# Performance work log

Hardware: AMD Instinct MI355X
Metric: run time of the kernel (lower is better)

Reference implementation:

```python
import jax, jax.numpy as jnp
import numpy as np

N = 50000        # num nodes
E = 1_600_000    # num edges
NNZ = 16         # sparse features per node
V = 100000       # feature vocabulary (num_total_features)
D = 128          # embedding_dim
H = 128          # hidden_dim
O = 64           # out_embedding_dim


def setup_inputs() -> dict:
    key = jax.random.key(0)
    ks = jax.random.split(key, 12)
    s = 0.05
    return {
        "feature_indices": jax.random.randint(ks[0], (N * NNZ,), 0, V, dtype=jnp.int32),
        "feature_offsets": jnp.arange(N, dtype=jnp.int32) * NNZ,
        "feature_weights": jax.random.uniform(ks[1], (N * NNZ,), dtype=jnp.float32),
        "edge_index": jax.random.randint(ks[2], (2, E), 0, N, dtype=jnp.int32),
        "noise": jax.random.normal(ks[3], (N, O), dtype=jnp.float32),
        "emb_table": jax.random.normal(ks[4], (V, D), dtype=jnp.float32) * s,
        "W1": jax.random.normal(ks[5], (D, H), dtype=jnp.float32) * s,
        "b1": jnp.zeros((H,), dtype=jnp.float32),
        "Wmu": jax.random.normal(ks[6], (H, O), dtype=jnp.float32) * s,
        "bmu": jnp.zeros((O,), dtype=jnp.float32),
        "Wls": jax.random.normal(ks[7], (H, O), dtype=jnp.float32) * s,
        "bls": jnp.zeros((O,), dtype=jnp.float32),
    }


def _gcn(x, W, b, src, dst, norm_e, deg_inv):
    # GCNConv with self-loops and symmetric normalization:
    # out_i = sum_{j->i} norm_ji * (W x_j) + deg_i^{-1} * (W x_i) + b
    xw = x @ W
    agg = jax.ops.segment_sum(norm_e[:, None] * xw[src], dst, num_segments=N)
    return agg + xw * deg_inv[:, None] + b


def reference(feature_indices, feature_offsets, feature_weights, edge_index, noise,
              emb_table, W1, b1, Wmu, bmu, Wls, bls):
    # --- EmbeddingBag(mode='sum') with per_sample_weights ---
    total = feature_indices.shape[0]
    bag_ids = jnp.searchsorted(feature_offsets, jnp.arange(total), side="right") - 1
    x = jax.ops.segment_sum(feature_weights[:, None] * emb_table[feature_indices],
                            bag_ids, num_segments=N)  # [N, D]
    # --- F.normalize(p=2, dim=-1) ---
    x = x / jnp.maximum(jnp.linalg.norm(x, axis=-1, keepdims=True), 1e-12)

    # --- shared GCN normalization (self-loops added) ---
    src, dst = edge_index[0], edge_index[1]
    deg = 1.0 + jax.ops.segment_sum(jnp.ones((E,), x.dtype), dst, num_segments=N)
    deg_isqrt = deg ** -0.5
    norm_e = deg_isqrt[src] * deg_isqrt[dst]  # per-edge norm
    deg_inv = 1.0 / deg                        # self-loop norm

    # --- encoder ---
    h = jax.nn.relu(_gcn(x, W1, b1, src, dst, norm_e, deg_inv))
    mu = _gcn(h, Wmu, bmu, src, dst, norm_e, deg_inv)
    logstd = _gcn(h, Wls, bls, src, dst, norm_e, deg_inv)
    z = mu + noise * jnp.exp(logstd)

    # --- dot-product decoder over edge_index ---
    logits = jnp.sum(z[src] * z[dst], axis=-1)  # [E]
    return logits
```

## Files before the change

### kernel.cpp

```cpp
#include <hip/hip_runtime.h>
#include <hip/hip_bf16.h>

constexpr int N_ = 50000;
constexpr int E_ = 1600000;
constexpr int D_ = 128;
constexpr int O_ = 64;
constexpr int NNZ_ = 16;
constexpr int V_ = 100000;
constexpr int NBIN_ = (N_ + 255) / 256;

static __device__ __forceinline__ unsigned short f2bf(float f) {
    __hip_bfloat16 h = __float2bfloat16(f);
    return __builtin_bit_cast(unsigned short, h);
}
static __device__ __forceinline__ unsigned int pack2(float a, float b) {
    return (unsigned int)f2bf(a) | ((unsigned int)f2bf(b) << 16);
}
static __device__ __forceinline__ float blo(unsigned int u) { return __uint_as_float(u << 16); }
static __device__ __forceinline__ float bhi(unsigned int u) { return __uint_as_float(u & 0xffff0000u); }
static __device__ __forceinline__ float4 fma4(float s, float4 a, float4 b) {
    return make_float4(fmaf(s, a.x, b.x), fmaf(s, a.y, b.y),
                       fmaf(s, a.z, b.z), fmaf(s, a.w, b.w));
}

__global__ __launch_bounds__(256) void k_cvt(const float* __restrict__ emb,
                                             unsigned int* __restrict__ emb_bf) {
    int t = blockIdx.x * blockDim.x + threadIdx.x;
    if (t >= V_ * D_ / 8) return;
    float4 a = ((const float4*)emb)[t * 2];
    float4 b = ((const float4*)emb)[t * 2 + 1];
    uint4 o;
    o.x = pack2(a.x, a.y);
    o.y = pack2(a.z, a.w);
    o.z = pack2(b.x, b.y);
    o.w = pack2(b.z, b.w);
    ((uint4*)emb_bf)[t] = o;
}

__global__ __launch_bounds__(256) void k_embed(const int* __restrict__ fi,
                                               const float* __restrict__ fw,
                                               const unsigned int* __restrict__ emb_bf,
                                               unsigned int* __restrict__ x) {
    int lane = threadIdx.x & 63;
    int h = lane >> 5, c = lane & 31;
    int n = blockIdx.x * 8 + ((threadIdx.x >> 6) << 1) + h;
    if (n >= N_) return;
    float a0 = 0.f, a1 = 0.f, a2 = 0.f, a3 = 0.f;
    int base = n * NNZ_;
#pragma unroll
    for (int j = 0; j < NNZ_; ++j) {
        int idx  = fi[base + j];
        float w  = fw[base + j];
        uint2 r = ((const uint2*)emb_bf)[(size_t)idx * 32 + c];
        a0 = fmaf(w, blo(r.x), a0);
        a1 = fmaf(w, bhi(r.x), a1);
        a2 = fmaf(w, blo(r.y), a2);
        a3 = fmaf(w, bhi(r.y), a3);
    }
    float ss = a0 * a0 + a1 * a1 + a2 * a2 + a3 * a3;
#pragma unroll
    for (int o = 16; o; o >>= 1) ss += __shfl_xor(ss, o);
    float sc = 1.0f / fmaxf(sqrtf(ss), 1e-12f);
    ((uint2*)x)[(size_t)n * 32 + c] =
        make_uint2(pack2(a0 * sc, a1 * sc), pack2(a2 * sc, a3 * sc));
}

constexpr int EPB_ = 8192;
__global__ __launch_bounds__(256) void k_bhist(const int* __restrict__ dst,
                                               int* __restrict__ bin_total) {
    __shared__ int hist[256];
    int t = threadIdx.x;
    hist[t] = 0;
    __syncthreads();
    int e0 = blockIdx.x * EPB_;
#pragma unroll
    for (int i = 0; i < EPB_ / 256; ++i) {
        int e = e0 + i * 256 + t;
        if (e < E_) atomicAdd(&hist[dst[e] >> 8], 1);
    }
    __syncthreads();
    if (t < NBIN_ && hist[t]) atomicAdd(&bin_total[t], hist[t]);
}

__global__ __launch_bounds__(256) void k_scan196(const int* __restrict__ bin_total,
                                                 int* __restrict__ coarse_start,
                                                 int* __restrict__ coarse_cursor,
                                                 int* __restrict__ row_start) {
    __shared__ int s[256];
    int t = threadIdx.x;
    int v = (t < NBIN_) ? bin_total[t] : 0;
    s[t] = v;
    __syncthreads();
    for (int o = 1; o < 256; o <<= 1) {
        int u = (t >= o) ? s[t - o] : 0;
        __syncthreads();
        s[t] += u;
        __syncthreads();
    }
    int excl = s[t] - v;
    if (t <= NBIN_) { coarse_start[t] = excl; coarse_cursor[t] = excl; }
    if (t == 0) row_start[N_] = E_;
}

__global__ __launch_bounds__(256) void k_bin(const int* __restrict__ src,
                                             const int* __restrict__ dst,
                                             int* __restrict__ coarse_cursor,
                                             unsigned int* __restrict__ binned) {
    __shared__ int hist[256], base[256];
    int t = threadIdx.x;
    int e0 = blockIdx.x * EPB_;
    hist[t] = 0;
    __syncthreads();
#pragma unroll
    for (int i = 0; i < EPB_ / 256; ++i) {
        int e = e0 + i * 256 + t;
        if (e < E_) atomicAdd(&hist[dst[e] >> 8], 1);
    }
    __syncthreads();
    if (t < NBIN_ && hist[t]) base[t] = atomicAdd(&coarse_cursor[t], hist[t]);
    __syncthreads();
#pragma unroll
    for (int i = 0; i < EPB_ / 256; ++i) {
        int e = e0 + i * 256 + t;
        if (e < E_) {
            int d = dst[e];
            int pos = atomicAdd(&base[d >> 8], 1);
            binned[pos] = (unsigned int)src[e] | ((unsigned int)(d & 255) << 16);
        }
    }
}

__global__ __launch_bounds__(256) void k_node(const unsigned int* __restrict__ binned,
                                              const int* __restrict__ coarse_start,
                                              float* __restrict__ disq,
                                              float* __restrict__ dinv,
                                              int* __restrict__ row_start) {
    __shared__ int hist[256], s[256];
    int t = threadIdx.x;
    hist[t] = 0;
    __syncthreads();
    int beg = coarse_start[blockIdx.x], end = coarse_start[blockIdx.x + 1];
    for (int j = beg + t; j < end; j += 256)
        atomicAdd(&hist[(binned[j] >> 16) & 255], 1);
    __syncthreads();
    int v = hist[t];
    int n = (blockIdx.x << 8) + t;
    if (n < N_) {
        float deg = 1.0f + (float)v;
        disq[n] = rsqrtf(deg);
        dinv[n] = 1.0f / deg;
    }
    s[t] = v;
    __syncthreads();
    for (int o = 1; o < 256; o <<= 1) {
        int u = (t >= o) ? s[t - o] : 0;
        __syncthreads();
        s[t] += u;
        __syncthreads();
    }
    if (n < N_) row_start[n] = beg + (s[t] - v);
}

__global__ __launch_bounds__(256) void k_fill2(const unsigned int* __restrict__ binned,
                                               const int* __restrict__ coarse_start,
                                               const int* __restrict__ row_start,
                                               int* __restrict__ sorted_src) {
    __shared__ int cur[256];
    int t = threadIdx.x;
    int n0 = blockIdx.x << 8;
    if (n0 + t < N_) cur[t] = row_start[n0 + t];
    __syncthreads();
    int beg = coarse_start[blockIdx.x], end = coarse_start[blockIdx.x + 1];
    for (int j = beg + t; j < end; j += 256) {
        unsigned int b = binned[j];
        int pos = atomicAdd(&cur[(b >> 16) & 255], 1);
        sorted_src[pos] = (int)(b & 0xFFFFu);
    }
}

__global__ __launch_bounds__(256) void k_gather(const int* __restrict__ row_start,
                                                const int* __restrict__ sorted_src,
                                                const float* __restrict__ disq,
                                                const float* __restrict__ dinv,
                                                const unsigned int* __restrict__ v,
                                                unsigned int* __restrict__ agg) {
    int n = blockIdx.x * 4 + (threadIdx.x >> 6);
    if (n >= N_) return;
    int lane = threadIdx.x & 63;
    int g = lane >> 4, c = lane & 15;
    const uint4* V = (const uint4*)v;
    int beg = row_start[n], end = row_start[n + 1];
    float a0 = 0.f, a1 = 0.f, a2 = 0.f, a3 = 0.f;
    float a4 = 0.f, a5 = 0.f, a6 = 0.f, a7 = 0.f;
    int j = beg;
    for (; j + 15 < end; j += 16) {
        int s0 = sorted_src[j      + g];
        int s1 = sorted_src[j + 4  + g];
        int s2 = sorted_src[j + 8  + g];
        int s3 = sorted_src[j + 12 + g];
        float w0 = disq[s0], w1 = disq[s1], w2 = disq[s2], w3 = disq[s3];
        uint4 b0 = V[(size_t)s0 * 16 + c];
        uint4 b1 = V[(size_t)s1 * 16 + c];
        uint4 b2 = V[(size_t)s2 * 16 + c];
        uint4 b3 = V[(size_t)s3 * 16 + c];
        a0 = fmaf(w0, blo(b0.x), a0); a1 = fmaf(w0, bhi(b0.x), a1);
        a2 = fmaf(w0, blo(b0.y), a2); a3 = fmaf(w0, bhi(b0.y), a3);
        a4 = fmaf(w0, blo(b0.z), a4); a5 = fmaf(w0, bhi(b0.z), a5);
        a6 = fmaf(w0, blo(b0.w), a6); a7 = fmaf(w0, bhi(b0.w), a7);
        a0 = fmaf(w1, blo(b1.x), a0); a1 = fmaf(w1, bhi(b1.x), a1);
        a2 = fmaf(w1, blo(b1.y), a2); a3 = fmaf(w1, bhi(b1.y), a3);
        a4 = fmaf(w1, blo(b1.z), a4); a5 = fmaf(w1, bhi(b1.z), a5);
        a6 = fmaf(w1, blo(b1.w), a6); a7 = fmaf(w1, bhi(b1.w), a7);
        a0 = fmaf(w2, blo(b2.x), a0); a1 = fmaf(w2, bhi(b2.x), a1);
        a2 = fmaf(w2, blo(b2.y), a2); a3 = fmaf(w2, bhi(b2.y), a3);
        a4 = fmaf(w2, blo(b2.z), a4); a5 = fmaf(w2, bhi(b2.z), a5);
        a6 = fmaf(w2, blo(b2.w), a6); a7 = fmaf(w2, bhi(b2.w), a7);
        a0 = fmaf(w3, blo(b3.x), a0); a1 = fmaf(w3, bhi(b3.x), a1);
        a2 = fmaf(w3, blo(b3.y), a2); a3 = fmaf(w3, bhi(b3.y), a3);
        a4 = fmaf(w3, blo(b3.z), a4); a5 = fmaf(w3, bhi(b3.z), a5);
        a6 = fmaf(w3, blo(b3.w), a6); a7 = fmaf(w3, bhi(b3.w), a7);
    }
    for (; j + g < end; j += 4) {
        int s = sorted_src[j + g];
        float w = disq[s];
        uint4 b = V[(size_t)s * 16 + c];
        a0 = fmaf(w, blo(b.x), a0); a1 = fmaf(w, bhi(b.x), a1);
        a2 = fmaf(w, blo(b.y), a2); a3 = fmaf(w, bhi(b.y), a3);
        a4 = fmaf(w, blo(b.z), a4); a5 = fmaf(w, bhi(b.z), a5);
        a6 = fmaf(w, blo(b.w), a6); a7 = fmaf(w, bhi(b.w), a7);
    }
    a0 += __shfl_xor(a0, 16); a0 += __shfl_xor(a0, 32);
    a1 += __shfl_xor(a1, 16); a1 += __shfl_xor(a1, 32);
    a2 += __shfl_xor(a2, 16); a2 += __shfl_xor(a2, 32);
    a3 += __shfl_xor(a3, 16); a3 += __shfl_xor(a3, 32);
    a4 += __shfl_xor(a4, 16); a4 += __shfl_xor(a4, 32);
    a5 += __shfl_xor(a5, 16); a5 += __shfl_xor(a5, 32);
    a6 += __shfl_xor(a6, 16); a6 += __shfl_xor(a6, 32);
    a7 += __shfl_xor(a7, 16); a7 += __shfl_xor(a7, 32);
    if (g == 0) {
        float dq = disq[n], di = dinv[n];
        uint4 bs = V[(size_t)n * 16 + c];
        a0 = fmaf(di, blo(bs.x), a0 * dq); a1 = fmaf(di, bhi(bs.x), a1 * dq);
        a2 = fmaf(di, blo(bs.y), a2 * dq); a3 = fmaf(di, bhi(bs.y), a3 * dq);
        a4 = fmaf(di, blo(bs.z), a4 * dq); a5 = fmaf(di, bhi(bs.z), a5 * dq);
        a6 = fmaf(di, blo(bs.w), a6 * dq); a7 = fmaf(di, bhi(bs.w), a7 * dq);
        ((uint4*)agg)[(size_t)n * 16 + c] =
            make_uint4(pack2(a0, a1), pack2(a2, a3), pack2(a4, a5), pack2(a6, a7));
    }
}

__global__ __launch_bounds__(256, 2) void k_gemm_relu(const unsigned int* __restrict__ ub,
                                                      const float* __restrict__ W,
                                                      const float* __restrict__ b,
                                                      unsigned short* __restrict__ hout) {
    __shared__ float lw[D_ * D_];
    __shared__ float lu[32 * D_];
    int tid = threadIdx.x;
    for (int t = tid; t < D_ * D_ / 4; t += 256)
        ((float4*)lw)[t] = ((const float4*)W)[t];

    int l  = tid & 31;
    int rl = ((tid >> 6) << 3) + (((tid >> 5) & 1) << 2);
    float4 bb = ((const float4*)b)[l];

    for (int tile = blockIdx.x; tile * 32 < N_; tile += gridDim.x) {
        int row0 = tile * 32;
        __syncthreads();
#pragma unroll
        for (int i = 0; i < 8; ++i) {
            int t = i * 256 + tid;
            int r = t >> 6, slot = t & 63;
            int gr = row0 + r;
            unsigned int bv = (gr < N_) ? ub[(size_t)gr * 64 + slot] : 0u;
            lu[r * D_ + slot * 2]     = blo(bv);
            lu[r * D_ + slot * 2 + 1] = bhi(bv);
        }
        __syncthreads();
        float4 a0 = {0,0,0,0}, a1 = {0,0,0,0}, a2 = {0,0,0,0}, a3 = {0,0,0,0};
#pragma unroll 4
        for (int k4 = 0; k4 < 32; ++k4) {
            int k = k4 * 4;
            float4 w0 = ((const float4*)(lw + (k + 0) * D_))[l];
            float4 w1 = ((const float4*)(lw + (k + 1) * D_))[l];
            float4 w2 = ((const float4*)(lw + (k + 2) * D_))[l];
            float4 w3 = ((const float4*)(lw + (k + 3) * D_))[l];
            float4 u0 = ((const float4*)(lu + (rl + 0) * D_))[k4];
            float4 u1 = ((const float4*)(lu + (rl + 1) * D_))[k4];
            float4 u2 = ((const float4*)(lu + (rl + 2) * D_))[k4];
            float4 u3 = ((const float4*)(lu + (rl + 3) * D_))[k4];
            a0 = fma4(u0.x, w0, fma4(u0.y, w1, fma4(u0.z, w2, fma4(u0.w, w3, a0))));
            a1 = fma4(u1.x, w0, fma4(u1.y, w1, fma4(u1.z, w2, fma4(u1.w, w3, a1))));
            a2 = fma4(u2.x, w0, fma4(u2.y, w1, fma4(u2.z, w2, fma4(u2.w, w3, a2))));
            a3 = fma4(u3.x, w0, fma4(u3.y, w1, fma4(u3.z, w2, fma4(u3.w, w3, a3))));
        }
        float4 accs[4] = {a0, a1, a2, a3};
#pragma unroll
        for (int r = 0; r < 4; ++r) {
            int row = row0 + rl + r;
            if (row < N_) {
                float4 a = accs[r];
                ushort4 o;
                o.x = f2bf(fmaxf(a.x + bb.x, 0.f));
                o.y = f2bf(fmaxf(a.y + bb.y, 0.f));
                o.z = f2bf(fmaxf(a.z + bb.z, 0.f));
                o.w = f2bf(fmaxf(a.w + bb.w, 0.f));
                ((ushort4*)hout)[(size_t)row * 32 + l] = o;
            }
        }
    }
}

__global__ __launch_bounds__(256, 2) void k_gemm_z(const unsigned int* __restrict__ gb,
                                                   const float* __restrict__ Wmu,
                                                   const float* __restrict__ bmu,
                                                   const float* __restrict__ Wls,
                                                   const float* __restrict__ bls,
                                                   const float* __restrict__ noise,
                                                   unsigned int* __restrict__ z) {
    __shared__ float lw[D_ * D_];
    __shared__ float lu[32 * D_];
    int tid = threadIdx.x;
    for (int t = tid; t < D_ * 32; t += 256) {
        int k = t >> 5, j2 = t & 31;
        float2 m2 = ((const float2*)Wmu)[k * 32 + j2];
        float2 l2 = ((const float2*)Wls)[k * 32 + j2];
        ((float4*)lw)[t] = make_float4(m2.x, l2.x, m2.y, l2.y);
    }

    int l  = tid & 31;
    int rl = ((tid >> 6) << 3) + (((tid >> 5) & 1) << 2);
    float2 bm = ((const float2*)bmu)[l];
    float2 bl = ((const float2*)bls)[l];
    float4 bb = make_float4(bm.x, bl.x, bm.y, bl.y);

    for (int tile = blockIdx.x; tile * 32 < N_; tile += gridDim.x) {
        int row0 = tile * 32;
        __syncthreads();
#pragma unroll
        for (int i = 0; i < 8; ++i) {
            int t = i * 256 + tid;
            int r = t >> 6, slot = t & 63;
            int gr = row0 + r;
            unsigned int bv = (gr < N_) ? gb[(size_t)gr * 64 + slot] : 0u;
            lu[r * D_ + slot * 2]     = blo(bv);
            lu[r * D_ + slot * 2 + 1] = bhi(bv);
        }
        __syncthreads();
        float4 a0 = {0,0,0,0}, a1 = {0,0,0,0}, a2 = {0,0,0,0}, a3 = {0,0,0,0};
#pragma unroll 4
        for (int k4 = 0; k4 < 32; ++k4) {
            int k = k4 * 4;
            float4 w0 = ((const float4*)(lw + (k + 0) * D_))[l];
            float4 w1 = ((const float4*)(lw + (k + 1) * D_))[l];
            float4 w2 = ((const float4*)(lw + (k + 2) * D_))[l];
            float4 w3 = ((const float4*)(lw + (k + 3) * D_))[l];
            float4 u0 = ((const float4*)(lu + (rl + 0) * D_))[k4];
            float4 u1 = ((const float4*)(lu + (rl + 1) * D_))[k4];
            float4 u2 = ((const float4*)(lu + (rl + 2) * D_))[k4];
            float4 u3 = ((const float4*)(lu + (rl + 3) * D_))[k4];
            a0 = fma4(u0.x, w0, fma4(u0.y, w1, fma4(u0.z, w2, fma4(u0.w, w3, a0))));
            a1 = fma4(u1.x, w0, fma4(u1.y, w1, fma4(u1.z, w2, fma4(u1.w, w3, a1))));
            a2 = fma4(u2.x, w0, fma4(u2.y, w1, fma4(u2.z, w2, fma4(u2.w, w3, a2))));
            a3 = fma4(u3.x, w0, fma4(u3.y, w1, fma4(u3.z, w2, fma4(u3.w, w3, a3))));
        }
        float4 accs[4] = {a0, a1, a2, a3};
#pragma unroll
        for (int r = 0; r < 4; ++r) {
            int row = row0 + rl + r;
            if (row < N_) {
                float4 a = accs[r];
                float2 n2 = ((const float2*)noise)[(size_t)row * 32 + l];
                float z0 = (a.x + bb.x) + n2.x * expf(a.y + bb.y);
                float z1 = (a.z + bb.z) + n2.y * expf(a.w + bb.w);
                z[(size_t)row * 32 + l] = pack2(z0, z1);
            }
        }
    }
}

__global__ __launch_bounds__(256) void k_decode(const int* __restrict__ src,
                                                const int* __restrict__ dst,
                                                const unsigned int* __restrict__ z,
                                                float* __restrict__ out) {
    int l = threadIdx.x & 7;
    int e0 = blockIdx.x * 128 + ((threadIdx.x >> 3) << 2);
    int s0 = src[e0],     d0 = dst[e0];
    int s1 = src[e0 + 1], d1 = dst[e0 + 1];
    int s2 = src[e0 + 2], d2 = dst[e0 + 2];
    int s3 = src[e0 + 3], d3 = dst[e0 + 3];
    const uint4* Z = (const uint4*)z;
    uint4 za0 = Z[(size_t)s0 * 8 + l], zb0 = Z[(size_t)d0 * 8 + l];
    uint4 za1 = Z[(size_t)s1 * 8 + l], zb1 = Z[(size_t)d1 * 8 + l];
    uint4 za2 = Z[(size_t)s2 * 8 + l], zb2 = Z[(size_t)d2 * 8 + l];
    uint4 za3 = Z[(size_t)s3 * 8 + l], zb3 = Z[(size_t)d3 * 8 + l];
    float p0 = blo(za0.x) * blo(zb0.x) + bhi(za0.x) * bhi(zb0.x)
             + blo(za0.y) * blo(zb0.y) + bhi(za0.y) * bhi(zb0.y)
             + blo(za0.z) * blo(zb0.z) + bhi(za0.z) * bhi(zb0.z)
             + blo(za0.w) * blo(zb0.w) + bhi(za0.w) * bhi(zb0.w);
    float p1 = blo(za1.x) * blo(zb1.x) + bhi(za1.x) * bhi(zb1.x)
             + blo(za1.y) * blo(zb1.y) + bhi(za1.y) * bhi(zb1.y)
             + blo(za1.z) * blo(zb1.z) + bhi(za1.z) * bhi(zb1.z)
             + blo(za1.w) * blo(zb1.w) + bhi(za1.w) * bhi(zb1.w);
    float p2 = blo(za2.x) * blo(zb2.x) + bhi(za2.x) * bhi(zb2.x)
             + blo(za2.y) * blo(zb2.y) + bhi(za2.y) * bhi(zb2.y)
             + blo(za2.z) * blo(zb2.z) + bhi(za2.z) * bhi(zb2.z)
             + blo(za2.w) * blo(zb2.w) + bhi(za2.w) * bhi(zb2.w);
    float p3 = blo(za3.x) * blo(zb3.x) + bhi(za3.x) * bhi(zb3.x)
             + blo(za3.y) * blo(zb3.y) + bhi(za3.y) * bhi(zb3.y)
             + blo(za3.z) * blo(zb3.z) + bhi(za3.z) * bhi(zb3.z)
             + blo(za3.w) * blo(zb3.w) + bhi(za3.w) * bhi(zb3.w);
#pragma unroll
    for (int o = 4; o; o >>= 1) {
        p0 += __shfl_xor(p0, o);
        p1 += __shfl_xor(p1, o);
        p2 += __shfl_xor(p2, o);
        p3 += __shfl_xor(p3, o);
    }
    if (l == 0) ((float4*)out)[e0 >> 2] = make_float4(p0, p1, p2, p3);
}

extern "C" void kernel_launch(void* const* d_in, const int* in_sizes, int n_in,
                              void* d_out, int out_size, void* d_ws, size_t ws_size,
                              hipStream_t stream) {
    const int*   fi    = (const int*)d_in[0];
    const float* fw    = (const float*)d_in[2];
    const int*   ei    = (const int*)d_in[3];
    const float* noise = (const float*)d_in[4];
    const float* emb   = (const float*)d_in[5];
    const float* W1    = (const float*)d_in[6];
    const float* b1    = (const float*)d_in[7];
    const float* Wmu   = (const float*)d_in[8];
    const float* bmu   = (const float*)d_in[9];
    const float* Wls   = (const float*)d_in[10];
    const float* bls   = (const float*)d_in[11];
    float* out = (float*)d_out;

    const int* src = ei;
    const int* dst = ei + E_;

    float*        ws        = (float*)d_ws;
    unsigned int* aggb      = (unsigned int*)ws;
    unsigned int* emb_bf    = (unsigned int*)ws;
    unsigned int* binned    = (unsigned int*)ws;
    unsigned int* x         = (unsigned int*)ws + (size_t)V_ * 64;
    unsigned int* h         = x + (size_t)N_ * 64;
    unsigned int* z         = h + (size_t)N_ * 64;
    float*        disq      = (float*)(z + (size_t)N_ * 32);
    float*        dinv      = disq + N_;
    int*          row_start = (int*)(dinv + N_);
    int*          sorted_src= row_start + (N_ + 1);
    int*          bin_total = sorted_src + E_;
    int*          coarse_start  = bin_total + 256;
    int*          coarse_cursor = coarse_start + 256;

    hipMemsetAsync(bin_total, 0, 256 * sizeof(int), stream);

    k_cvt    <<<(V_ * D_ / 8 + 255) / 256, 256, 0, stream>>>(emb, emb_bf);
    k_embed  <<<(N_ + 7) / 8,           256, 0, stream>>>(fi, fw, emb_bf, x);
    k_bhist  <<<(E_ + EPB_ - 1) / EPB_, 256, 0, stream>>>(dst, bin_total);
    k_scan196<<<1,                      256, 0, stream>>>(bin_total, coarse_start,
                                                          coarse_cursor, row_start);
    k_bin    <<<(E_ + EPB_ - 1) / EPB_, 256, 0, stream>>>(src, dst, coarse_cursor, binned);
    k_node   <<<NBIN_,                  256, 0, stream>>>(binned, coarse_start,
                                                          disq, dinv, row_start);
    k_fill2  <<<NBIN_,                  256, 0, stream>>>(binned, coarse_start,
                                                          row_start, sorted_src);

    k_gather   <<<N_ / 4, 256, 0, stream>>>(row_start, sorted_src, disq, dinv, x, aggb);
    k_gemm_relu<<<512,    256, 0, stream>>>(aggb, W1, b1, (unsigned short*)h);

    k_gather <<<N_ / 4,   256, 0, stream>>>(row_start, sorted_src, disq, dinv, h, aggb);
    k_gemm_z <<<512,      256, 0, stream>>>(aggb, Wmu, bmu, Wls, bls, noise, z);

    k_decode <<<E_ / 128, 256, 0, stream>>>(src, dst, z, out);
}
```

Baseline: 445.0 us.

## Reuse per-block histograms in binning, fuse node/fill kernels, deepen gather unroll

k_bhist now stores each block's 256-bin histogram in workspace, so k_bin reads it instead of recomputing the histogram with a second pass over dst. k_node and k_fill2 are merged into one kernel that keeps the row-start cursor in shared memory, which removes a launch and a row_start re-read. The gather kernel gains a 32-edge unrolled loop that issues 8 independent row loads per thread for more memory-level parallelism. The cost is extra workspace for the block histograms and higher register pressure in the gather kernel.

```diff
diff --git a/kernel.cpp b/kernel.cpp
--- a/kernel.cpp
+++ b/kernel.cpp
@@ -67,7 +67,8 @@
 
 constexpr int EPB_ = 8192;
 __global__ __launch_bounds__(256) void k_bhist(const int* __restrict__ dst,
-                                               int* __restrict__ bin_total) {
+                                               int* __restrict__ bin_total,
+                                               int* __restrict__ blk_hist) {
     __shared__ int hist[256];
     int t = threadIdx.x;
     hist[t] = 0;
@@ -79,7 +80,9 @@
         if (e < E_) atomicAdd(&hist[dst[e] >> 8], 1);
     }
     __syncthreads();
-    if (t < NBIN_ && hist[t]) atomicAdd(&bin_total[t], hist[t]);
+    int v = hist[t];
+    blk_hist[blockIdx.x * 256 + t] = v;
+    if (t < NBIN_ && v) atomicAdd(&bin_total[t], v);
 }
 
 __global__ __launch_bounds__(256) void k_scan196(const int* __restrict__ bin_total,
@@ -104,21 +107,15 @@
 
 __global__ __launch_bounds__(256) void k_bin(const int* __restrict__ src,
                                              const int* __restrict__ dst,
+                                             const int* __restrict__ blk_hist,
                                              int* __restrict__ coarse_cursor,
                                              unsigned int* __restrict__ binned) {
-    __shared__ int hist[256], base[256];
+    __shared__ int base[256];
     int t = threadIdx.x;
+    int hv = blk_hist[blockIdx.x * 256 + t];
+    if (t < NBIN_ && hv) base[t] = atomicAdd(&coarse_cursor[t], hv);
+    __syncthreads();
     int e0 = blockIdx.x * EPB_;
-    hist[t] = 0;
-    __syncthreads();
-#pragma unroll
-    for (int i = 0; i < EPB_ / 256; ++i) {
-        int e = e0 + i * 256 + t;
-        if (e < E_) atomicAdd(&hist[dst[e] >> 8], 1);
-    }
-    __syncthreads();
-    if (t < NBIN_ && hist[t]) base[t] = atomicAdd(&coarse_cursor[t], hist[t]);
-    __syncthreads();
 #pragma unroll
     for (int i = 0; i < EPB_ / 256; ++i) {
         int e = e0 + i * 256 + t;
@@ -130,12 +127,13 @@
     }
 }
 
-__global__ __launch_bounds__(256) void k_node(const unsigned int* __restrict__ binned,
-                                              const int* __restrict__ coarse_start,
-                                              float* __restrict__ disq,
-                                              float* __restrict__ dinv,
-                                              int* __restrict__ row_start) {
-    __shared__ int hist[256], s[256];
+__global__ __launch_bounds__(256) void k_nodefill(const unsigned int* __restrict__ binned,
+                                                  const int* __restrict__ coarse_start,
+                                                  float* __restrict__ disq,
+                                                  float* __restrict__ dinv,
+                                                  int* __restrict__ row_start,
+                                                  int* __restrict__ sorted_src) {
+    __shared__ int hist[256], s[256], cur[256];
     int t = threadIdx.x;
     hist[t] = 0;
     __syncthreads();
@@ -158,19 +156,10 @@
         s[t] += u;
         __syncthreads();
     }
-    if (n < N_) row_start[n] = beg + (s[t] - v);
-}
-
-__global__ __launch_bounds__(256) void k_fill2(const unsigned int* __restrict__ binned,
-                                               const int* __restrict__ coarse_start,
-                                               const int* __restrict__ row_start,
-                                               int* __restrict__ sorted_src) {
-    __shared__ int cur[256];
-    int t = threadIdx.x;
-    int n0 = blockIdx.x << 8;
-    if (n0 + t < N_) cur[t] = row_start[n0 + t];
-    __syncthreads();
-    int beg = coarse_start[blockIdx.x], end = coarse_start[blockIdx.x + 1];
+    int rs = beg + (s[t] - v);
+    if (n < N_) row_start[n] = rs;
+    cur[t] = rs;
+    __syncthreads();
     for (int j = beg + t; j < end; j += 256) {
         unsigned int b = binned[j];
         int pos = atomicAdd(&cur[(b >> 16) & 255], 1);
@@ -193,37 +182,42 @@
     float a0 = 0.f, a1 = 0.f, a2 = 0.f, a3 = 0.f;
     float a4 = 0.f, a5 = 0.f, a6 = 0.f, a7 = 0.f;
     int j = beg;
+    for (; j + 31 < end; j += 32) {
+        int ss[8]; float ww[8]; uint4 bb[8];
+#pragma unroll
+        for (int q = 0; q < 8; ++q) ss[q] = sorted_src[j + 4 * q + g];
+#pragma unroll
+        for (int q = 0; q < 8; ++q) ww[q] = disq[ss[q]];
+#pragma unroll
+        for (int q = 0; q < 8; ++q) bb[q] = V[(size_t)ss[q] * 16 + c];
+#pragma unroll
+        for (int q = 0; q < 8; ++q) {
+            a0 = fmaf(ww[q], blo(bb[q].x), a0); a1 = fmaf(ww[q], bhi(bb[q].x), a1);
+            a2 = fmaf(ww[q], blo(bb[q].y), a2); a3 = fmaf(ww[q], bhi(bb[q].y), a3);
+            a4 = fmaf(ww[q], blo(bb[q].z), a4); a5 = fmaf(ww[q], bhi(bb[q].z), a5);
+            a6 = fmaf(ww[q], blo(bb[q].w), a6); a7 = fmaf(ww[q], bhi(bb[q].w), a7);
+        }
+    }
     for (; j + 15 < end; j += 16) {
-        int s0 = sorted_src[j      + g];
-        int s1 = sorted_src[j + 4  + g];
-        int s2 = sorted_src[j + 8  + g];
-        int s3 = sorted_src[j + 12 + g];
-        float w0 = disq[s0], w1 = disq[s1], w2 = disq[s2], w3 = disq[s3];
-        uint4 b0 = V[(size_t)s0 * 16 + c];
-        uint4 b1 = V[(size_t)s1 * 16 + c];
-        uint4 b2 = V[(size_t)s2 * 16 + c];
-        uint4 b3 = V[(size_t)s3 * 16 + c];
-        a0 = fmaf(w0, blo(b0.x), a0); a1 = fmaf(w0, bhi(b0.x), a1);
-        a2 = fmaf(w0, blo(b0.y), a2); a3 = fmaf(w0, bhi(b0.y), a3);
-        a4 = fmaf(w0, blo(b0.z), a4); a5 = fmaf(w0, bhi(b0.z), a5);
-        a6 = fmaf(w0, blo(b0.w), a6); a7 = fmaf(w0, bhi(b0.w), a7);
-        a0 = fmaf(w1, blo(b1.x), a0); a1 = fmaf(w1, bhi(b1.x), a1);
-        a2 = fmaf(w1, blo(b1.y), a2); a3 = fmaf(w1, bhi(b1.y), a3);
-        a4 = fmaf(w1, blo(b1.z), a4); a5 = fmaf(w1, bhi(b1.z), a5);
-        a6 = fmaf(w1, blo(b1.w), a6); a7 = fmaf(w1, bhi(b1.w), a7);
-        a0 = fmaf(w2, blo(b2.x), a0); a1 = fmaf(w2, bhi(b2.x), a1);
-        a2 = fmaf(w2, blo(b2.y), a2); a3 = fmaf(w2, bhi(b2.y), a3);
-        a4 = fmaf(w2, blo(b2.z), a4); a5 = fmaf(w2, bhi(b2.z), a5);
-        a6 = fmaf(w2, blo(b2.w), a6); a7 = fmaf(w2, bhi(b2.w), a7);
-        a0 = fmaf(w3, blo(b3.x), a0); a1 = fmaf(w3, bhi(b3.x), a1);
-        a2 = fmaf(w3, blo(b3.y), a2); a3 = fmaf(w3, bhi(b3.y), a3);
-        a4 = fmaf(w3, blo(b3.z), a4); a5 = fmaf(w3, bhi(b3.z), a5);
-        a6 = fmaf(w3, blo(b3.w), a6); a7 = fmaf(w3, bhi(b3.w), a7);
+        int ss[4]; float ww[4]; uint4 bb[4];
+#pragma unroll
+        for (int q = 0; q < 4; ++q) ss[q] = sorted_src[j + 4 * q + g];
+#pragma unroll
+        for (int q = 0; q < 4; ++q) ww[q] = disq[ss[q]];
+#pragma unroll
+        for (int q = 0; q < 4; ++q) bb[q] = V[(size_t)ss[q] * 16 + c];
+#pragma unroll
+        for (int q = 0; q < 4; ++q) {
+            a0 = fmaf(ww[q], blo(bb[q].x), a0); a1 = fmaf(ww[q], bhi(bb[q].x), a1);
+            a2 = fmaf(ww[q], blo(bb[q].y), a2); a3 = fmaf(ww[q], bhi(bb[q].y), a3);
+            a4 = fmaf(ww[q], blo(bb[q].z), a4); a5 = fmaf(ww[q], bhi(bb[q].z), a5);
+            a6 = fmaf(ww[q], blo(bb[q].w), a6); a7 = fmaf(ww[q], bhi(bb[q].w), a7);
+        }
     }
     for (; j + g < end; j += 4) {
-        int s = sorted_src[j + g];
-        float w = disq[s];
-        uint4 b = V[(size_t)s * 16 + c];
+        int s0 = sorted_src[j + g];
+        float w = disq[s0];
+        uint4 b = V[(size_t)s0 * 16 + c];
         a0 = fmaf(w, blo(b.x), a0); a1 = fmaf(w, bhi(b.x), a1);
         a2 = fmaf(w, blo(b.y), a2); a3 = fmaf(w, bhi(b.y), a3);
         a4 = fmaf(w, blo(b.z), a4); a5 = fmaf(w, bhi(b.z), a5);
@@ -452,19 +446,21 @@
     int*          bin_total = sorted_src + E_;
     int*          coarse_start  = bin_total + 256;
     int*          coarse_cursor = coarse_start + 256;
+    int*          blk_hist  = coarse_cursor + 256;
+
+    const int nblk = (E_ + EPB_ - 1) / EPB_;
 
     hipMemsetAsync(bin_total, 0, 256 * sizeof(int), stream);
 
     k_cvt    <<<(V_ * D_ / 8 + 255) / 256, 256, 0, stream>>>(emb, emb_bf);
-    k_embed  <<<(N_ + 7) / 8,           256, 0, stream>>>(fi, fw, emb_bf, x);
-    k_bhist  <<<(E_ + EPB_ - 1) / EPB_, 256, 0, stream>>>(dst, bin_total);
-    k_scan196<<<1,                      256, 0, stream>>>(bin_total, coarse_start,
-                                                          coarse_cursor, row_start);
-    k_bin    <<<(E_ + EPB_ - 1) / EPB_, 256, 0, stream>>>(src, dst, coarse_cursor, binned);
-    k_node   <<<NBIN_,                  256, 0, stream>>>(binned, coarse_start,
-                                                          disq, dinv, row_start);
-    k_fill2  <<<NBIN_,                  256, 0, stream>>>(binned, coarse_start,
-                                                          row_start, sorted_src);
+    k_embed  <<<(N_ + 7) / 8, 256, 0, stream>>>(fi, fw, emb_bf, x);
+    k_bhist  <<<nblk,         256, 0, stream>>>(dst, bin_total, blk_hist);
+    k_scan196<<<1,            256, 0, stream>>>(bin_total, coarse_start,
+                                                coarse_cursor, row_start);
+    k_bin    <<<nblk,         256, 0, stream>>>(src, dst, blk_hist,
+                                                coarse_cursor, binned);
+    k_nodefill<<<NBIN_,       256, 0, stream>>>(binned, coarse_start,
+                                                disq, dinv, row_start, sorted_src);
 
     k_gather   <<<N_ / 4, 256, 0, stream>>>(row_start, sorted_src, disq, dinv, x, aggb);
     k_gemm_relu<<<512,    256, 0, stream>>>(aggb, W1, b1, (unsigned short*)h);
```

After: 465.1 us. +4.5%, slower.
